# Performance work log

Measured on AMD Instinct MI355X. Metric: run time of the kernel, lower is better.

Reference implementation:

```python
import jax, jax.numpy as jnp
import numpy as np

NUM_HEADS = 16
ROPE_BASE = 50.0


def _apply_rope(x):
    # x: [b, s, h, d]; torchtune-style rotary embedding with base=ROPE_BASE
    b, s, h, d = x.shape
    inv_freq = 1.0 / (ROPE_BASE ** (jnp.arange(0, d, 2, dtype=jnp.float32) / d))  # [d/2]
    angles = jnp.arange(s, dtype=jnp.float32)[:, None] * inv_freq[None, :]         # [s, d/2]
    cos = jnp.cos(angles)[None, :, None, :]  # [1, s, 1, d/2]
    sin = jnp.sin(angles)[None, :, None, :]
    xr = x.reshape(b, s, h, d // 2, 2)
    x0, x1 = xr[..., 0], xr[..., 1]
    out = jnp.stack([x0 * cos - x1 * sin, x1 * cos + x0 * sin], axis=-1)
    return out.reshape(b, s, h, d).astype(x.dtype)


def setup_inputs() -> dict:
    key = jax.random.key(0)
    k1, k2, k3 = jax.random.split(key, 3)
    B, S, D = 2, 2048, 1024
    x = jax.random.normal(k1, (B, S, D), dtype=jnp.float32)
    w_qkv = jax.random.normal(k2, (3 * D, D), dtype=jnp.float32) * (D ** -0.5)
    w_out = jax.random.normal(k3, (D, D), dtype=jnp.float32) * (D ** -0.5)
    b_out = jnp.zeros((D,), dtype=jnp.float32)
    return {"x": x, "w_qkv": w_qkv, "w_out": w_out, "b_out": b_out}


def reference(x, w_qkv, w_out, b_out):
    B, S, D = x.shape
    H = NUM_HEADS
    dk = D // H

    qkv = x @ w_qkv.T                       # [b, s, 3D]
    q, k, v = jnp.split(qkv, 3, axis=-1)
    q = q.reshape(B, S, H, dk)
    k = k.reshape(B, S, H, dk)
    q = _apply_rope(q)
    k = _apply_rope(k)
    q = q.transpose(0, 2, 1, 3)             # [b, h, s, d]
    k = k.transpose(0, 2, 1, 3)
    v = v.reshape(B, S, H, dk).transpose(0, 2, 1, 3)

    scale = 1.0 / jnp.sqrt(jnp.asarray(dk, dtype=x.dtype))
    scores = jnp.einsum('bhsd,bhtd->bhst', q, k) * scale  # [b, h, s, s]
    # additive diagonal mask: -inf on the diagonal (blocks self-attention)
    eye = jnp.eye(S, dtype=bool)
    scores = jnp.where(eye[None, None], -jnp.inf, scores)
    attn = jax.nn.softmax(scores, axis=-1)
    out = jnp.einsum('bhst,bhtd->bhsd', attn, v)          # [b, h, s, d]
    out = out.transpose(0, 2, 1, 3).reshape(B, S, D)
    return out @ w_out.T + b_out
```

## Files before the change

### kernel.cpp

```cpp
#include <hip/hip_runtime.h>
#include <hip/hip_bf16.h>
#include <math.h>
#include <type_traits>

#define D_MODEL 1024
#define NHEADS  16
#define DK      64
#define SEQ     2048
#define BATCH   2
#define QTILE   128

typedef __attribute__((ext_vector_type(8)))  short  short8;
typedef __attribute__((ext_vector_type(8)))  unsigned short ushort8;
typedef __attribute__((ext_vector_type(4)))  float  floatx4;
typedef __attribute__((ext_vector_type(16))) float  floatx16;

__device__ __forceinline__ unsigned short f2bf(float f) {
    union { float f; unsigned int u; } v; v.f = f;
    unsigned int u = v.u;
    return (unsigned short)((u + 0x7FFFu + ((u >> 16) & 1u)) >> 16);
}
__device__ __forceinline__ float bf2f(unsigned short u) {
    union { unsigned int u; float f; } v; v.u = ((unsigned int)u) << 16;
    return v.f;
}
__device__ __forceinline__ unsigned int fau(float f) {
    union { float f; unsigned int u; } v; v.f = f; return v.u;
}

__device__ __forceinline__ void gload_lds16(const unsigned short* g, unsigned short* l) {
    __builtin_amdgcn_global_load_lds((__attribute__((address_space(1))) const void*)g,
                                     (__attribute__((address_space(3))) void*)l,
                                     16, 0, 0);
}

#define X8 ((BATCH * SEQ * D_MODEL) / 8)
#define W8 ((3 * D_MODEL * D_MODEL) / 8)
#define O8 ((D_MODEL * D_MODEL) / 8)
__global__ __launch_bounds__(256) void pack_all(const float* __restrict__ x,
                                                const float* __restrict__ wq,
                                                const float* __restrict__ wo,
                                                unsigned short* __restrict__ xb,
                                                unsigned short* __restrict__ wqb,
                                                unsigned short* __restrict__ wob) {
    const int t = blockIdx.x * blockDim.x + threadIdx.x;
    const float* src; unsigned short* dst; int idx;
    if (t < X8)           { src = x;  dst = xb;  idx = t; }
    else if (t < X8 + W8) { src = wq; dst = wqb; idx = t - X8; }
    else if (t < X8 + W8 + O8) { src = wo; dst = wob; idx = t - X8 - W8; }
    else return;
    const float4 a = ((const float4*)src)[2 * idx];
    const float4 b = ((const float4*)src)[2 * idx + 1];
    short8 o;
    o[0] = (short)f2bf(a.x); o[1] = (short)f2bf(a.y);
    o[2] = (short)f2bf(a.z); o[3] = (short)f2bf(a.w);
    o[4] = (short)f2bf(b.x); o[5] = (short)f2bf(b.y);
    o[6] = (short)f2bf(b.z); o[7] = (short)f2bf(b.w);
    ((short8*)dst)[idx] = o;
}

template <int TM, typename OUT_T>
__global__ __launch_bounds__(256) void gemm_bf16(const unsigned short* __restrict__ A,
                                                 const unsigned short* __restrict__ B,
                                                 const float* __restrict__ bias,
                                                 OUT_T* __restrict__ C,
                                                 int M, int N, int K) {
    constexpr int NAF = TM / 32;
    __shared__ __align__(16) unsigned short As[TM][32];
    __shared__ __align__(16) unsigned short Bs[128][32];

    const int tid  = threadIdx.x;
    const int wave = tid >> 6;
    const int lane = tid & 63;
    const int quad = lane >> 4;
    const int lcol = lane & 15;
    const int wr   = (wave >> 1) * (TM / 2);
    const int wc   = (wave & 1) * 64;
    const int tm   = blockIdx.y * TM;
    const int tn   = blockIdx.x * 128;

    const int srowA = wave * (TM / 4) + (lane >> 2);
    const int srowB = wave * 32 + (lane >> 2);
    const int scol  = (lane & 3) * 8;
    const unsigned short* gB0 = B + (size_t)(tn + srowB) * K + scol;
    const unsigned short* gB1 = gB0 + (size_t)16 * K;
    unsigned short* lB0 = &Bs[wave * 32][0];
    unsigned short* lB1 = &Bs[wave * 32 + 16][0];

    floatx4 acc[NAF][4];
#pragma unroll
    for (int i = 0; i < NAF; ++i)
#pragma unroll
        for (int j = 0; j < 4; ++j) acc[i][j] = (floatx4){0.f, 0.f, 0.f, 0.f};

    for (int k0 = 0; k0 < K; k0 += 32) {
        __syncthreads();
#pragma unroll
        for (int u = 0; u < TM / 64; ++u)
            gload_lds16(A + (size_t)(tm + srowA + u * 16) * K + k0 + scol,
                        &As[wave * (TM / 4) + u * 16][0]);
        gload_lds16(gB0 + k0, lB0);
        gload_lds16(gB1 + k0, lB1);
        __syncthreads();

        short8 af[NAF], bf[4];
#pragma unroll
        for (int i = 0; i < NAF; ++i) af[i] = *(short8*)&As[wr + i * 16 + lcol][quad * 8];
#pragma unroll
        for (int j = 0; j < 4; ++j) bf[j] = *(short8*)&Bs[wc + j * 16 + lcol][quad * 8];
#pragma unroll
        for (int i = 0; i < NAF; ++i)
#pragma unroll
            for (int j = 0; j < 4; ++j)
                acc[i][j] = __builtin_amdgcn_mfma_f32_16x16x32_bf16(af[i], bf[j], acc[i][j], 0, 0, 0);
    }

#pragma unroll
    for (int i = 0; i < NAF; ++i) {
#pragma unroll
        for (int r = 0; r < 4; ++r) {
            const int row = tm + wr + i * 16 + quad * 4 + r;
#pragma unroll
            for (int j = 0; j < 4; ++j) {
                const int col = tn + wc + j * 16 + lcol;
                float v = acc[i][j][r];
                if (bias) v += bias[col];
                if constexpr (sizeof(OUT_T) == 2)
                    C[(size_t)row * N + col] = (OUT_T)f2bf(v);
                else
                    C[(size_t)row * N + col] = (OUT_T)v;
            }
        }
    }
}

#define QKV_M 4096
#define QKV_N 3072
#define QKV_K 1024
#define QKV_NT (QKV_K / 64)

__global__ __launch_bounds__(512, 2) void gemm_qkv_8ph(const unsigned short* __restrict__ A,
                                                        const unsigned short* __restrict__ B,
                                                        unsigned short* __restrict__ C) {
    __shared__ __align__(16) unsigned short As[2][256][64];
    __shared__ __align__(16) unsigned short Bs[2][256][64];

    const int tid  = threadIdx.x;
    const int w    = tid >> 6;
    const int lane = tid & 63;
    const int quad = lane >> 4;
    const int lcol = lane & 15;
    const int wr   = w >> 2;
    const int wc   = w & 3;

    const int f  = blockIdx.x;
    const int wg = (f & 7) * 24 + (f >> 3);
    const int tn = (wg % (QKV_N / 256)) * 256;
    const int tm = (wg / (QKV_N / 256)) * 256;

    const int srow8 = lane >> 3;
    const int sj    = lane & 7;

    auto stageA = [&](int buf, int kt, int mh) {
#pragma unroll
        for (int c = 0; c < 2; ++c) {
            const int r0 = mh * 64 + c * 128 + w * 8;
            const int r  = r0 + srow8;
            gload_lds16(A + (size_t)(tm + r) * QKV_K + kt * 64 + ((sj ^ (r & 7)) * 8),
                        &As[buf][r0][0]);
        }
    };
    auto stageB = [&](int buf, int kt, int nh) {
#pragma unroll
        for (int c = 0; c < 2; ++c) {
            const int rho0 = c * 64 + w * 8;
            const int r0   = (rho0 >> 5) * 64 + nh * 32 + (rho0 & 31);
            const int r    = r0 + srow8;
            gload_lds16(B + (size_t)(tn + r) * QKV_K + kt * 64 + ((sj ^ (r & 7)) * 8),
                        &Bs[buf][r0][0]);
        }
    };

    floatx4 acc[8][4];
#pragma unroll
    for (int i = 0; i < 8; ++i)
#pragma unroll
        for (int j = 0; j < 4; ++j) acc[i][j] = (floatx4){0.f, 0.f, 0.f, 0.f};

    auto do_phase = [&](int buf, auto mhc, auto nhc, auto stager) {
        constexpr int mh = decltype(mhc)::value;
        constexpr int nh = decltype(nhc)::value;
        asm volatile("s_waitcnt vmcnt(4)" ::: "memory");
        __builtin_amdgcn_s_barrier();
        asm volatile("" ::: "memory");
        short8 a[4][2], bfr[2][2];
#pragma unroll
        for (int i = 0; i < 4; ++i)
#pragma unroll
            for (int kk = 0; kk < 2; ++kk) {
                const int r = wr * 128 + mh * 64 + i * 16 + lcol;
                a[i][kk] = *(const short8*)&As[buf][r][((kk * 4 + quad) ^ (r & 7)) * 8];
            }
#pragma unroll
        for (int j = 0; j < 2; ++j)
#pragma unroll
            for (int kk = 0; kk < 2; ++kk) {
                const int r = wc * 64 + nh * 32 + j * 16 + lcol;
                bfr[j][kk] = *(const short8*)&Bs[buf][r][((kk * 4 + quad) ^ (r & 7)) * 8];
            }
        stager();
        __builtin_amdgcn_s_setprio(1);
#pragma unroll
        for (int i = 0; i < 4; ++i)
#pragma unroll
            for (int j = 0; j < 2; ++j)
#pragma unroll
                for (int kk = 0; kk < 2; ++kk)
                    acc[mh * 4 + i][nh * 2 + j] = __builtin_amdgcn_mfma_f32_16x16x32_bf16(
                        a[i][kk], bfr[j][kk], acc[mh * 4 + i][nh * 2 + j], 0, 0, 0);
        __builtin_amdgcn_s_setprio(0);
    };

    using IC0 = std::integral_constant<int, 0>;
    using IC1 = std::integral_constant<int, 1>;

    stageA(0, 0, 0); stageB(0, 0, 0); stageB(0, 0, 1); stageA(0, 0, 1);

    for (int t = 0; t < QKV_NT; ++t) {
        const int buf = t & 1, nb = buf ^ 1;
        const int kn = (t + 1 == QKV_NT) ? 0 : t + 1;
        do_phase(buf, IC0{}, IC0{}, [&] { stageA(nb, kn, 0); });
        do_phase(buf, IC0{}, IC1{}, [&] { stageB(nb, kn, 0); });
        do_phase(buf, IC1{}, IC0{}, [&] { stageB(nb, kn, 1); });
        do_phase(buf, IC1{}, IC1{}, [&] { stageA(nb, kn, 1); });
    }

#pragma unroll
    for (int i = 0; i < 8; ++i) {
#pragma unroll
        for (int rr = 0; rr < 4; ++rr) {
            const int row = tm + wr * 128 + i * 16 + quad * 4 + rr;
#pragma unroll
            for (int jf = 0; jf < 4; ++jf) {
                const int col = tn + wc * 64 + jf * 16 + lcol;
                C[(size_t)row * QKV_N + col] = f2bf(acc[i][jf][rr]);
            }
        }
    }
}

__global__ __launch_bounds__(256) void rope_vtrans(const unsigned short* __restrict__ qkvb,
                                                   unsigned short* __restrict__ Qb,
                                                   unsigned short* __restrict__ Kb,
                                                   unsigned short* __restrict__ Vtg) {
    const int st = blockIdx.x, h = blockIdx.y, b = blockIdx.z;
    const int tid = threadIdx.x;
    const int s0 = st * 64;

    const int i  = tid & 31;
    const int r0 = tid >> 5;
    const float inv_freq = exp2f(-(2.0f * (float)i / (float)DK) * log2f(50.0f));
    const float QSCALE = 0.125f * 1.44269504f;
#pragma unroll
    for (int pass = 0; pass < 8; ++pass) {
        const int s = s0 + r0 + pass * 8;
        const size_t in_base = ((size_t)(b * SEQ + s)) * (3 * D_MODEL) + h * DK + 2 * i;
        const float q0 = bf2f(qkvb[in_base]),           q1 = bf2f(qkvb[in_base + 1]);
        const float k0 = bf2f(qkvb[in_base + D_MODEL]), k1 = bf2f(qkvb[in_base + D_MODEL + 1]);
        float sn, cs;
        __sincosf((float)s * inv_freq, &sn, &cs);
        const size_t ob = (((size_t)(b * NHEADS + h)) * SEQ + s) * DK + 2 * i;
        const unsigned int qw = (unsigned int)f2bf((q0 * cs - q1 * sn) * QSCALE)
                              | ((unsigned int)f2bf((q1 * cs + q0 * sn) * QSCALE) << 16);
        const unsigned int kw = (unsigned int)f2bf(k0 * cs - k1 * sn)
                              | ((unsigned int)f2bf(k1 * cs + k0 * sn) << 16);
        *(unsigned int*)&Qb[ob] = qw;
        *(unsigned int*)&Kb[ob] = kw;
    }

    __shared__ unsigned short Lt[64][65];
    const int r = tid >> 3;
    const int c = (tid & 7) * 8;
    const size_t in_row = ((size_t)(b * SEQ + s0 + r)) * (3 * D_MODEL) + 2 * D_MODEL + h * DK + c;
    const ushort8 v0 = *(const ushort8*)&qkvb[in_row];
    const ushort8 v1 = *(const ushort8*)&qkvb[in_row + (size_t)32 * (3 * D_MODEL)];
    const int u0 = r, u1 = r + 32;
    const int kc0 = (u0 & 48) | (8 * ((u0 >> 2) & 1) + (u0 & 3) + 4 * ((u0 >> 3) & 1));
    const int kc1 = (u1 & 48) | (8 * ((u1 >> 2) & 1) + (u1 & 3) + 4 * ((u1 >> 3) & 1));
#pragma unroll
    for (int j = 0; j < 8; ++j) Lt[c + j][kc0] = v0[j];
#pragma unroll
    for (int j = 0; j < 8; ++j) Lt[c + j][kc1] = v1[j];
    __syncthreads();
    const size_t bh = (size_t)(b * NHEADS + h);
    ushort8 o0, o1;
#pragma unroll
    for (int j = 0; j < 8; ++j) { o0[j] = Lt[r][c + j]; o1[j] = Lt[r + 32][c + j]; }
    unsigned short* orow = Vtg + (bh * DK + r) * SEQ + s0 + c;
    *(ushort8*)orow = o0;
    *(ushort8*)(orow + (size_t)32 * SEQ) = o1;
}

#define LDW 72

__global__ __launch_bounds__(512, 4) void flash_attn(const unsigned short* __restrict__ Qb,
                                                     const unsigned short* __restrict__ Kb,
                                                     const unsigned short* __restrict__ Vtg,
                                                     unsigned short* __restrict__ attnb) {
    const int tid  = threadIdx.x;
    const int wave = tid >> 6;
    const int lane = tid & 63;
    const int l31  = lane & 31;
    const int lh   = lane >> 5;
    const int mh2  = wave & 3;
    const int kh   = wave >> 2;
    const int kb   = kh * 32;

    const int f  = blockIdx.x + gridDim.x * (blockIdx.y + gridDim.y * blockIdx.z);
    const int w  = (f & 7) * 64 + (f >> 3);
    const int qt = w & 15;
    const int h  = (w >> 4) & 15;
    const int b  = w >> 8;

    __shared__ __align__(16) unsigned char smem[36864];
    unsigned short (*Ks0)[LDW] = (unsigned short (*)[LDW])(smem);
    unsigned short (*Vt0)[LDW] = (unsigned short (*)[LDW])(smem +  9216);
    unsigned short (*Ks1)[LDW] = (unsigned short (*)[LDW])(smem + 18432);
    unsigned short (*Vt1)[LDW] = (unsigned short (*)[LDW])(smem + 27648);
    float (*Ored)[68] = (float (*)[68])smem;
    float* lred0 = (float*)(smem + 34816);
    float* lred1 = lred0 + 128;

    const size_t bh = (size_t)(b * NHEADS + h);
    const unsigned short* Qg = Qb + (bh * SEQ + (size_t)qt * QTILE) * DK;
    const unsigned short* Kg = Kb + bh * SEQ * DK;
    const unsigned short* Vg = Vtg + bh * (size_t)DK * SEQ;

    short8 qf[4];
#pragma unroll
    for (int t = 0; t < 4; ++t)
        qf[t] = *(const short8*)&Qg[(size_t)(mh2 * 32 + l31) * DK + t * 16 + lh * 8];

    const int strow = tid >> 3;
    const int stcol = (tid & 7) * 8;
    const unsigned short* kg = &Kg[(size_t)strow * DK + stcol];
    const unsigned short* vg = &Vg[(size_t)strow * SEQ + stcol];

    short8 kr = *(const short8*)&kg[0];
    short8 vr = *(const short8*)&vg[0];

    floatx16 oacc[2];
    oacc[0] = (floatx16)(0.f);
    oacc[1] = (floatx16)(0.f);
    float lp = 0.f;

    const int diagkt = qt * QTILE + mh2 * 32 - kb;

    auto compute = [&](unsigned short (*Ks)[LDW], unsigned short (*Vt)[LDW], int kt) {
        floatx16 sc = (floatx16)(0.f);
        __builtin_amdgcn_s_setprio(1);
#pragma unroll
        for (int t = 0; t < 4; ++t) {
            const short8 kf = *(short8*)&Ks[kb + l31][t * 16 + lh * 8];
            sc = __builtin_amdgcn_mfma_f32_32x32x16_bf16(kf, qf[t], sc, 0, 0, 0);
        }
        __builtin_amdgcn_s_setprio(0);

        if (kt == diagkt) {
#pragma unroll
            for (int r = 0; r < 16; ++r) {
                const int key_loc = (r & 3) + 8 * (r >> 2) + 4 * lh;
                if (key_loc == l31) sc[r] = -1e30f;
            }
        }

        short8 pf0, pf1;
        {
            union { unsigned int u[4]; short8 s8; } a, c;
#pragma unroll
            for (int d = 0; d < 4; ++d) {
                const float e0 = __builtin_amdgcn_exp2f(sc[2 * d]);
                const float e1 = __builtin_amdgcn_exp2f(sc[2 * d + 1]);
                a.u[d] = __builtin_amdgcn_perm(fau(e1), fau(e0), 0x07060302u);
                const float f0 = __builtin_amdgcn_exp2f(sc[8 + 2 * d]);
                const float f1 = __builtin_amdgcn_exp2f(sc[8 + 2 * d + 1]);
                c.u[d] = __builtin_amdgcn_perm(fau(f1), fau(f0), 0x07060302u);
                lp += (e0 + e1) + (f0 + f1);
            }
            pf0 = a.s8;
            pf1 = c.s8;
        }

        __builtin_amdgcn_s_setprio(1);
#pragma unroll
        for (int nd = 0; nd < 2; ++nd) {
            const short8 vfa = *(short8*)&Vt[nd * 32 + l31][kb + lh * 8];
            const short8 vfb = *(short8*)&Vt[nd * 32 + l31][kb + 16 + lh * 8];
            oacc[nd] = __builtin_amdgcn_mfma_f32_32x32x16_bf16(pf0, vfa, oacc[nd], 0, 0, 0);
            oacc[nd] = __builtin_amdgcn_mfma_f32_32x32x16_bf16(pf1, vfb, oacc[nd], 0, 0, 0);
        }
        __builtin_amdgcn_s_setprio(0);
    };

    for (int kt = 0; kt < SEQ; kt += 128) {
        *(short8*)&Ks0[strow][stcol] = kr;
        *(short8*)&Vt0[strow][stcol] = vr;
        __syncthreads();
        kr = *(const short8*)&kg[(size_t)(kt + 64) * DK];
        vr = *(const short8*)&vg[kt + 64];
        compute(Ks0, Vt0, kt);

        *(short8*)&Ks1[strow][stcol] = kr;
        *(short8*)&Vt1[strow][stcol] = vr;
        __syncthreads();
        const int ktn = (kt + 128 < SEQ) ? kt + 128 : 0;
        kr = *(const short8*)&kg[(size_t)ktn * DK];
        vr = *(const short8*)&vg[ktn];
        compute(Ks1, Vt1, kt + 64);
    }

    const float lptot = lp + __shfl_xor(lp, 32, 64);

    __syncthreads();
    if (lh == 0) {
        if (kh == 0) lred0[mh2 * 32 + l31] = lptot;
        else         lred1[mh2 * 32 + l31] = lptot;
    }
    if (kh == 1) {
#pragma unroll
        for (int r = 0; r < 16; ++r) {
            const int m = mh2 * 32 + (r & 3) + 8 * (r >> 2) + 4 * lh;
            Ored[m][l31]      = oacc[0][r];
            Ored[m][32 + l31] = oacc[1][r];
        }
    }
    __syncthreads();
    if (kh == 0) {
        unsigned short* obase = attnb + ((size_t)b * SEQ + (size_t)qt * QTILE) * D_MODEL + h * DK;
#pragma unroll
        for (int r = 0; r < 16; ++r) {
            const int m = mh2 * 32 + (r & 3) + 8 * (r >> 2) + 4 * lh;
            const float inv = 1.001953125f / (lred0[m] + lred1[m]);
            const float v0 = (oacc[0][r] + Ored[m][l31]) * inv;
            const float v1 = (oacc[1][r] + Ored[m][32 + l31]) * inv;
            obase[(size_t)m * D_MODEL + l31]      = f2bf(v0);
            obase[(size_t)m * D_MODEL + 32 + l31] = f2bf(v1);
        }
    }
}

extern "C" void kernel_launch(void* const* d_in, const int* in_sizes, int n_in,
                              void* d_out, int out_size, void* d_ws, size_t ws_size,
                              hipStream_t stream) {
    const float* x     = (const float*)d_in[0];
    const float* w_qkv = (const float*)d_in[1];
    const float* w_out = (const float*)d_in[2];
    const float* b_out = (const float*)d_in[3];
    float* out = (float*)d_out;

    const int M = BATCH * SEQ;
    const size_t X_ELEMS    = (size_t)M * D_MODEL;
    const size_t WQKV_ELEMS = (size_t)3 * D_MODEL * D_MODEL;
    const size_t WOUT_ELEMS = (size_t)D_MODEL * D_MODEL;
    const size_t QKV_ELEMS  = (size_t)M * 3 * D_MODEL;
    const size_t HEAD_ELEMS = (size_t)BATCH * NHEADS * SEQ * DK;

    unsigned short* xb    = (unsigned short*)d_ws;
    unsigned short* wqkvb = xb + X_ELEMS;
    unsigned short* woutb = wqkvb + WQKV_ELEMS;
    unsigned short* qkvb  = woutb + WOUT_ELEMS;
    unsigned short* Qb    = qkvb + QKV_ELEMS;
    unsigned short* Kb    = Qb + HEAD_ELEMS;
    unsigned short* Vtg   = Kb + HEAD_ELEMS;
    unsigned short* attnb = Vtg + HEAD_ELEMS;

    pack_all<<<(X8 + W8 + O8 + 255) / 256, 256, 0, stream>>>(x, w_qkv, w_out, xb, wqkvb, woutb);

    gemm_qkv_8ph<<<(QKV_M / 256) * (QKV_N / 256), 512, 0, stream>>>(xb, wqkvb, qkvb);

    {
        dim3 grid(SEQ / 64, NHEADS, BATCH);
        rope_vtrans<<<grid, 256, 0, stream>>>(qkvb, Qb, Kb, Vtg);
    }
    {
        dim3 grid(SEQ / QTILE, NHEADS, BATCH);
        flash_attn<<<grid, 512, 0, stream>>>(Qb, Kb, Vtg, attnb);
    }
    {
        dim3 grid(D_MODEL / 128, M / 64);
        gemm_bf16<64, float><<<grid, 256, 0, stream>>>(attnb, woutb, b_out, out,
                                                       M, D_MODEL, D_MODEL);
    }
}
```

Before: 186.7 us.

## Replace output projection GEMM with double-buffered 8-wave phased kernel

Replaces the generic single-buffered gemm_bf16 used for the output projection with a specialised 128x128-tile kernel of 512 threads. It double-buffers LDS and splits each K step into four phases that interleave the next tile's global-to-LDS loads with MFMA work. It also adds an XOR swizzle to avoid LDS bank conflicts and a remapped block order for L2 locality. The aim is to hide memory latency and synchronisation stalls. The cost is more LDS per block and a kernel hardcoded to these shapes.

Measured after the change: 185.0 us. No clear change (-0.9%).

```diff
diff --git a/kernel.cpp b/kernel.cpp
--- a/kernel.cpp
+++ b/kernel.cpp
@@ -59,81 +59,6 @@
     ((short8*)dst)[idx] = o;
 }
 
-template <int TM, typename OUT_T>
-__global__ __launch_bounds__(256) void gemm_bf16(const unsigned short* __restrict__ A,
-                                                 const unsigned short* __restrict__ B,
-                                                 const float* __restrict__ bias,
-                                                 OUT_T* __restrict__ C,
-                                                 int M, int N, int K) {
-    constexpr int NAF = TM / 32;
-    __shared__ __align__(16) unsigned short As[TM][32];
-    __shared__ __align__(16) unsigned short Bs[128][32];
-
-    const int tid  = threadIdx.x;
-    const int wave = tid >> 6;
-    const int lane = tid & 63;
-    const int quad = lane >> 4;
-    const int lcol = lane & 15;
-    const int wr   = (wave >> 1) * (TM / 2);
-    const int wc   = (wave & 1) * 64;
-    const int tm   = blockIdx.y * TM;
-    const int tn   = blockIdx.x * 128;
-
-    const int srowA = wave * (TM / 4) + (lane >> 2);
-    const int srowB = wave * 32 + (lane >> 2);
-    const int scol  = (lane & 3) * 8;
-    const unsigned short* gB0 = B + (size_t)(tn + srowB) * K + scol;
-    const unsigned short* gB1 = gB0 + (size_t)16 * K;
-    unsigned short* lB0 = &Bs[wave * 32][0];
-    unsigned short* lB1 = &Bs[wave * 32 + 16][0];
-
-    floatx4 acc[NAF][4];
-#pragma unroll
-    for (int i = 0; i < NAF; ++i)
-#pragma unroll
-        for (int j = 0; j < 4; ++j) acc[i][j] = (floatx4){0.f, 0.f, 0.f, 0.f};
-
-    for (int k0 = 0; k0 < K; k0 += 32) {
-        __syncthreads();
-#pragma unroll
-        for (int u = 0; u < TM / 64; ++u)
-            gload_lds16(A + (size_t)(tm + srowA + u * 16) * K + k0 + scol,
-                        &As[wave * (TM / 4) + u * 16][0]);
-        gload_lds16(gB0 + k0, lB0);
-        gload_lds16(gB1 + k0, lB1);
-        __syncthreads();
-
-        short8 af[NAF], bf[4];
-#pragma unroll
-        for (int i = 0; i < NAF; ++i) af[i] = *(short8*)&As[wr + i * 16 + lcol][quad * 8];
-#pragma unroll
-        for (int j = 0; j < 4; ++j) bf[j] = *(short8*)&Bs[wc + j * 16 + lcol][quad * 8];
-#pragma unroll
-        for (int i = 0; i < NAF; ++i)
-#pragma unroll
-            for (int j = 0; j < 4; ++j)
-                acc[i][j] = __builtin_amdgcn_mfma_f32_16x16x32_bf16(af[i], bf[j], acc[i][j], 0, 0, 0);
-    }
-
-#pragma unroll
-    for (int i = 0; i < NAF; ++i) {
-#pragma unroll
-        for (int r = 0; r < 4; ++r) {
-            const int row = tm + wr + i * 16 + quad * 4 + r;
-#pragma unroll
-            for (int j = 0; j < 4; ++j) {
-                const int col = tn + wc + j * 16 + lcol;
-                float v = acc[i][j][r];
-                if (bias) v += bias[col];
-                if constexpr (sizeof(OUT_T) == 2)
-                    C[(size_t)row * N + col] = (OUT_T)f2bf(v);
-                else
-                    C[(size_t)row * N + col] = (OUT_T)v;
-            }
-        }
-    }
-}
-
 #define QKV_M 4096
 #define QKV_N 3072
 #define QKV_K 1024
@@ -244,6 +169,111 @@
             for (int jf = 0; jf < 4; ++jf) {
                 const int col = tn + wc * 64 + jf * 16 + lcol;
                 C[(size_t)row * QKV_N + col] = f2bf(acc[i][jf][rr]);
+            }
+        }
+    }
+}
+
+#define OUT_M 4096
+#define OUT_N 1024
+#define OUT_K 1024
+#define OUT_NT (OUT_K / 64)
+
+__global__ __launch_bounds__(512, 2) void gemm_out_8ph(const unsigned short* __restrict__ A,
+                                                       const unsigned short* __restrict__ B,
+                                                       const float* __restrict__ bias,
+                                                       float* __restrict__ C) {
+    __shared__ __align__(16) unsigned short As[2][128][64];
+    __shared__ __align__(16) unsigned short Bs[2][128][64];
+
+    const int tid  = threadIdx.x;
+    const int w    = tid >> 6;
+    const int lane = tid & 63;
+    const int quad = lane >> 4;
+    const int lcol = lane & 15;
+    const int wr   = w >> 2;
+    const int wc   = w & 3;
+
+    const int f  = blockIdx.x;
+    const int wg = (f & 7) * 32 + (f >> 3);
+    const int tn = (wg & 7) * 128;
+    const int tm = (wg >> 3) * 128;
+
+    const int srow8 = lane >> 3;
+    const int sj    = lane & 7;
+
+    auto stageA = [&](int buf, int kt, int mh) {
+        const int r0 = (w & 3) * 8 + mh * 32 + (w >> 2) * 64;
+        const int r  = r0 + srow8;
+        gload_lds16(A + (size_t)(tm + r) * OUT_K + kt * 64 + ((sj ^ (r & 7)) * 8),
+                    &As[buf][r0][0]);
+    };
+    auto stageB = [&](int buf, int kt, int nh) {
+        const int r0 = (w >> 1) * 32 + nh * 16 + (w & 1) * 8;
+        const int r  = r0 + srow8;
+        gload_lds16(B + (size_t)(tn + r) * OUT_K + kt * 64 + ((sj ^ (r & 7)) * 8),
+                    &Bs[buf][r0][0]);
+    };
+
+    floatx4 acc[4][2];
+#pragma unroll
+    for (int i = 0; i < 4; ++i)
+#pragma unroll
+        for (int j = 0; j < 2; ++j) acc[i][j] = (floatx4){0.f, 0.f, 0.f, 0.f};
+
+    auto do_phase = [&](int buf, auto mhc, auto nhc, auto stager) {
+        constexpr int mh = decltype(mhc)::value;
+        constexpr int nh = decltype(nhc)::value;
+        asm volatile("s_waitcnt vmcnt(2)" ::: "memory");
+        __builtin_amdgcn_s_barrier();
+        asm volatile("" ::: "memory");
+        short8 a[2][2], bfr[2];
+#pragma unroll
+        for (int i = 0; i < 2; ++i)
+#pragma unroll
+            for (int kk = 0; kk < 2; ++kk) {
+                const int r = wr * 64 + mh * 32 + i * 16 + lcol;
+                a[i][kk] = *(const short8*)&As[buf][r][((kk * 4 + quad) ^ (r & 7)) * 8];
+            }
+#pragma unroll
+        for (int kk = 0; kk < 2; ++kk) {
+            const int r = wc * 32 + nh * 16 + lcol;
+            bfr[kk] = *(const short8*)&Bs[buf][r][((kk * 4 + quad) ^ (r & 7)) * 8];
+        }
+        stager();
+        __builtin_amdgcn_s_setprio(1);
+#pragma unroll
+        for (int i = 0; i < 2; ++i)
+#pragma unroll
+            for (int kk = 0; kk < 2; ++kk)
+                acc[mh * 2 + i][nh] = __builtin_amdgcn_mfma_f32_16x16x32_bf16(
+                    a[i][kk], bfr[kk], acc[mh * 2 + i][nh], 0, 0, 0);
+        __builtin_amdgcn_s_setprio(0);
+    };
+
+    using IC0 = std::integral_constant<int, 0>;
+    using IC1 = std::integral_constant<int, 1>;
+
+    stageA(0, 0, 0); stageB(0, 0, 0); stageB(0, 0, 1); stageA(0, 0, 1);
+
+    for (int t = 0; t < OUT_NT; ++t) {
+        const int buf = t & 1, nb = buf ^ 1;
+        const int kn = (t + 1 == OUT_NT) ? 0 : t + 1;
+        do_phase(buf, IC0{}, IC0{}, [&] { stageA(nb, kn, 0); });
+        do_phase(buf, IC0{}, IC1{}, [&] { stageB(nb, kn, 0); });
+        do_phase(buf, IC1{}, IC0{}, [&] { stageB(nb, kn, 1); });
+        do_phase(buf, IC1{}, IC1{}, [&] { stageA(nb, kn, 1); });
+    }
+
+#pragma unroll
+    for (int i = 0; i < 4; ++i) {
+#pragma unroll
+        for (int rr = 0; rr < 4; ++rr) {
+            const int row = tm + wr * 64 + i * 16 + quad * 4 + rr;
+#pragma unroll
+            for (int j = 0; j < 2; ++j) {
+                const int col = tn + wc * 32 + j * 16 + lcol;
+                C[(size_t)row * OUT_N + col] = acc[i][j][rr] + bias[col];
             }
         }
     }
@@ -486,9 +516,5 @@
         dim3 grid(SEQ / QTILE, NHEADS, BATCH);
         flash_attn<<<grid, 512, 0, stream>>>(Qb, Kb, Vtg, attnb);
     }
-    {
-        dim3 grid(D_MODEL / 128, M / 64);
-        gemm_bf16<64, float><<<grid, 256, 0, stream>>>(attnb, woutb, b_out, out,
-                                                       M, D_MODEL, D_MODEL);
-    }
-}
+    gemm_out_8ph<<<(OUT_M / 128) * (OUT_N / 128), 512, 0, stream>>>(attnb, woutb, b_out, out);
+}
```
